# Kernel optimization log

Measured on AMD Instinct MI355X. Metric: run time of the kernel, lower is better.

Reference implementation:

```python
import jax, jax.numpy as jnp
import numpy as np

B, T, C = 4, 2048, 1024
HEAD = 2048

def setup_inputs() -> dict:
    key = jax.random.key(0)
    ks = jax.random.split(key, 7)
    s = 1.0 / np.sqrt(C)
    return {
        "x":  jax.random.normal(ks[0], (B, T, C), dtype=jnp.float32),
        "Wq": jax.random.uniform(ks[1], (C, HEAD), dtype=jnp.float32, minval=-s, maxval=s),
        "bq": jax.random.uniform(ks[2], (HEAD,), dtype=jnp.float32, minval=-s, maxval=s),
        "Wk": jax.random.uniform(ks[3], (C, HEAD), dtype=jnp.float32, minval=-s, maxval=s),
        "bk": jax.random.uniform(ks[4], (HEAD,), dtype=jnp.float32, minval=-s, maxval=s),
        "Wv": jax.random.uniform(ks[5], (C, HEAD), dtype=jnp.float32, minval=-s, maxval=s),
        "bv": jax.random.uniform(ks[6], (HEAD,), dtype=jnp.float32, minval=-s, maxval=s),
    }

def reference(x, Wq, bq, Wk, bk, Wv, bv):
    # q,k,v: [B,T,HEAD]
    q = jnp.einsum('btc,ch->bth', x, Wq) + bq
    k = jnp.einsum('btc,ch->bth', x, Wk) + bk
    v = jnp.einsum('btc,ch->bth', x, Wv) + bv
    scale = x.shape[-1] ** -0.5  # NOTE: original scales by n_embed**-0.5, not head_size
    wei = jnp.einsum('bth,bsh->bts', q, k) * scale  # [B,T,T]
    Tn = x.shape[1]
    causal = jnp.tril(jnp.ones((Tn, Tn), dtype=bool))
    wei = jnp.where(causal, wei, -jnp.inf)
    wei = jax.nn.softmax(wei, axis=-1)
    # dropout is identity in eval mode
    out = jnp.einsum('bts,bsh->bth', wei, v)  # [B,T,HEAD]
    return out
```

## Files before the change

kernel.cpp:

```cpp
#include <hip/hip_runtime.h>


#define T_    2048
#define C_    1024
#define B_    4
#define NQK   4096
#define SCALE 0.03125f

typedef __attribute__((ext_vector_type(4))) float floatx4;
typedef __attribute__((ext_vector_type(8))) short short8;
typedef __attribute__((ext_vector_type(8))) unsigned short ushortx8;

__device__ __forceinline__ unsigned short f2bf(float f) {
  unsigned int u = __float_as_uint(f);
  unsigned int r = (u + 0x7fffu + ((u >> 16) & 1u)) >> 16;
  return (unsigned short)r;
}

__global__ void cast_x_kernel(const float* __restrict__ x, ushort* __restrict__ xbf) {
  int i = blockIdx.x * 256 + threadIdx.x;
  float4 v = ((const float4*)x)[i];
  ushort4 o;
  o.x = f2bf(v.x); o.y = f2bf(v.y); o.z = f2bf(v.z); o.w = f2bf(v.w);
  ((ushort4*)xbf)[i] = o;
}

__global__ void wcast_t_kernel(const float* __restrict__ Wq, const float* __restrict__ Wk,
                               const float* __restrict__ Wv, ushort* __restrict__ WtT) {
  int k0 = blockIdx.x * 32;
  int n0 = blockIdx.y * 32;
  const float* W = (n0 < 2048) ? Wq : (n0 < 4096 ? Wk : Wv);
  int nl0 = n0 & 2047;
  __shared__ ushort tile[32][33];
  int tx = threadIdx.x, ty = threadIdx.y;
  for (int r = ty; r < 32; r += 8)
    tile[r][tx] = f2bf(W[(size_t)(k0 + r) * 2048 + nl0 + tx]);
  __syncthreads();
  for (int r = ty; r < 32; r += 8)
    WtT[(size_t)(n0 + r) * 1024 + k0 + tx] = tile[tx][r];
}

__global__ void bias_cat_kernel(const float* __restrict__ bq, const float* __restrict__ bk,
                                const float* __restrict__ bv, float* __restrict__ bcat) {
  int i = blockIdx.x * 256 + threadIdx.x;
  if (i < 6144) {
    const float* s = (i < 2048) ? bq : (i < 4096 ? bk : bv);
    bcat[i] = s[i & 2047];
  }
}

__device__ __forceinline__ void stage128x32(const ushort* g, int ld, char* lds,
                                            int wave, int lane) {
#pragma unroll
  for (int c = 0; c < 2; ++c) {
    int chunk = wave + 4 * c;
    const ushort* gaddr = g + (size_t)(chunk * 16 + (lane >> 2)) * ld + (lane & 3) * 8;
    char* laddr = lds + chunk * 1024;
    __builtin_amdgcn_global_load_lds((const __attribute__((address_space(1))) unsigned int*)gaddr,
                                     (__attribute__((address_space(3))) unsigned int*)laddr,
                                     16, 0, 0);
  }
}

__device__ __forceinline__ void gemm_core(const ushort* A, int lda,
                                          const ushort* Bm, int ldb, int ksteps,
                                          char* ldsA, char* ldsB, floatx4 acc[4][4]) {
  int tid = threadIdx.x;
  int wave = tid >> 6, lane = tid & 63;
  int wm = wave >> 1, wn = wave & 1;
  int koff2 = ((lane >> 4) * 8) * 2;
  int rbase = lane & 15;
  for (int s = 0; s < ksteps; ++s) {
    __syncthreads();
    stage128x32(A + s * 32, lda, ldsA, wave, lane);
    stage128x32(Bm + s * 32, ldb, ldsB, wave, lane);
    __syncthreads();
    short8 af[4], bf[4];
#pragma unroll
    for (int i = 0; i < 4; ++i) {
      af[i] = *(const short8*)(ldsA + (wm * 64 + i * 16 + rbase) * 64 + koff2);
      bf[i] = *(const short8*)(ldsB + (wn * 64 + i * 16 + rbase) * 64 + koff2);
    }
#pragma unroll
    for (int i = 0; i < 4; ++i)
#pragma unroll
      for (int j = 0; j < 4; ++j)
        acc[i][j] = __builtin_amdgcn_mfma_f32_16x16x32_bf16(af[i], bf[j], acc[i][j], 0, 0, 0);
  }
}


#define MFMA16(a, b, c) __builtin_amdgcn_mfma_f32_16x16x32_bf16((a), (b), (c), 0, 0, 0)

#define GLDS16(gsrc, ldst)                                                                       \
  __builtin_amdgcn_global_load_lds((const __attribute__((address_space(1))) unsigned int*)(gsrc), \
                                   (__attribute__((address_space(3))) unsigned int*)(ldst), 16, 0, 0)
#define STAGE2(gsrc, ldst) do { GLDS16((gsrc), (ldst)); GLDS16((gsrc) + 8192, (ldst) + 1024); } while (0)

#define PHASE_MID() do {                                   \
  __builtin_amdgcn_sched_barrier(0);                       \
  __builtin_amdgcn_s_barrier();                            \
  asm volatile("s_waitcnt lgkmcnt(0)" ::: "memory");       \
  __builtin_amdgcn_sched_barrier(0);                       \
  __builtin_amdgcn_s_setprio(1);                           \
} while (0)

#define PHASE_END() do {                                   \
  __builtin_amdgcn_s_setprio(0);                           \
  __builtin_amdgcn_sched_barrier(0);                       \
  __builtin_amdgcn_s_barrier();                            \
  __builtin_amdgcn_sched_barrier(0);                       \
} while (0)

template <bool TAIL>
__device__ __forceinline__ void iter_qk(const ushort* __restrict__ Ap,
                                        const ushort* __restrict__ Bp,
                                        char* lds, int kt0, int wave, int wm, int wn,
                                        int srcOff, int lnoff0, floatx4 (&acc)[8][4]) {
  char* rA0 = lds + wm * 16384;
  char* rA1 = rA0 + 32768;
  char* rB0 = lds + 65536 + (wn >> 1) * 16384 + (wn & 1) * 8192;
  char* rB1 = rB0 + 32768;
  const ushort* sA1 = Ap + (kt0 + 1) * 64 + srcOff;
  const ushort* sA2 = Ap + (kt0 + 2) * 64 + srcOff;
  const ushort* sB2 = Bp + (kt0 + 2) * 64 + srcOff;
  const ushort* sB3 = Bp + (kt0 + 3) * 64 + srcOff;
  const int lnoff1 = lnoff0 ^ 64;
  short8 af[4][2], blo[2][2], bhi[2][2];

#pragma unroll
  for (int mi = 0; mi < 4; ++mi) {
    af[mi][0] = *(const short8*)(rA0 + mi * 2048 + lnoff0);
    af[mi][1] = *(const short8*)(rA0 + mi * 2048 + lnoff1);
  }
#pragma unroll
  for (int nj = 0; nj < 2; ++nj) {
    blo[nj][0] = *(const short8*)(rB0 + nj * 2048 + lnoff0);
    blo[nj][1] = *(const short8*)(rB0 + nj * 2048 + lnoff1);
  }
  STAGE2(sA1, lds + 32768 + wave * 2048);
  PHASE_MID();
#pragma unroll
  for (int mi = 0; mi < 4; ++mi)
#pragma unroll
    for (int nj = 0; nj < 2; ++nj) {
      acc[mi][nj] = MFMA16(af[mi][0], blo[nj][0], acc[mi][nj]);
      acc[mi][nj] = MFMA16(af[mi][1], blo[nj][1], acc[mi][nj]);
    }
  PHASE_END();

#pragma unroll
  for (int nj = 0; nj < 2; ++nj) {
    bhi[nj][0] = *(const short8*)(rB0 + (2 + nj) * 2048 + lnoff0);
    bhi[nj][1] = *(const short8*)(rB0 + (2 + nj) * 2048 + lnoff1);
  }
  STAGE2(sA1 + 131072, lds + 49152 + wave * 2048);
  PHASE_MID();
#pragma unroll
  for (int mi = 0; mi < 4; ++mi)
#pragma unroll
    for (int nj = 0; nj < 2; ++nj) {
      acc[mi][2 + nj] = MFMA16(af[mi][0], bhi[nj][0], acc[mi][2 + nj]);
      acc[mi][2 + nj] = MFMA16(af[mi][1], bhi[nj][1], acc[mi][2 + nj]);
    }
  PHASE_END();

#pragma unroll
  for (int mi = 0; mi < 4; ++mi) {
    af[mi][0] = *(const short8*)(rA0 + (4 + mi) * 2048 + lnoff0);
    af[mi][1] = *(const short8*)(rA0 + (4 + mi) * 2048 + lnoff1);
  }
  if constexpr (!TAIL) STAGE2(sB2, lds + 65536 + wave * 2048);
  PHASE_MID();
#pragma unroll
  for (int mi = 0; mi < 4; ++mi)
#pragma unroll
    for (int nj = 0; nj < 2; ++nj) {
      acc[4 + mi][2 + nj] = MFMA16(af[mi][0], bhi[nj][0], acc[4 + mi][2 + nj]);
      acc[4 + mi][2 + nj] = MFMA16(af[mi][1], bhi[nj][1], acc[4 + mi][2 + nj]);
    }
  PHASE_END();

  if constexpr (!TAIL) STAGE2(sB2 + 131072, lds + 81920 + wave * 2048);
  PHASE_MID();
#pragma unroll
  for (int mi = 0; mi < 4; ++mi)
#pragma unroll
    for (int nj = 0; nj < 2; ++nj) {
      acc[4 + mi][nj] = MFMA16(af[mi][0], blo[nj][0], acc[4 + mi][nj]);
      acc[4 + mi][nj] = MFMA16(af[mi][1], blo[nj][1], acc[4 + mi][nj]);
    }
  __builtin_amdgcn_s_setprio(0);
  __builtin_amdgcn_sched_barrier(0);
  if constexpr (TAIL) asm volatile("s_waitcnt vmcnt(0)" ::: "memory");
  else                asm volatile("s_waitcnt vmcnt(4)" ::: "memory");
  __builtin_amdgcn_sched_barrier(0);
  __builtin_amdgcn_s_barrier();
  __builtin_amdgcn_sched_barrier(0);

#pragma unroll
  for (int mi = 0; mi < 4; ++mi) {
    af[mi][0] = *(const short8*)(rA1 + mi * 2048 + lnoff0);
    af[mi][1] = *(const short8*)(rA1 + mi * 2048 + lnoff1);
  }
#pragma unroll
  for (int nj = 0; nj < 2; ++nj) {
    blo[nj][0] = *(const short8*)(rB1 + nj * 2048 + lnoff0);
    blo[nj][1] = *(const short8*)(rB1 + nj * 2048 + lnoff1);
  }
  if constexpr (!TAIL) STAGE2(sA2, lds + wave * 2048);
  PHASE_MID();
#pragma unroll
  for (int mi = 0; mi < 4; ++mi)
#pragma unroll
    for (int nj = 0; nj < 2; ++nj) {
      acc[mi][nj] = MFMA16(af[mi][0], blo[nj][0], acc[mi][nj]);
      acc[mi][nj] = MFMA16(af[mi][1], blo[nj][1], acc[mi][nj]);
    }
  PHASE_END();

#pragma unroll
  for (int nj = 0; nj < 2; ++nj) {
    bhi[nj][0] = *(const short8*)(rB1 + (2 + nj) * 2048 + lnoff0);
    bhi[nj][1] = *(const short8*)(rB1 + (2 + nj) * 2048 + lnoff1);
  }
  if constexpr (!TAIL) STAGE2(sA2 + 131072, lds + 16384 + wave * 2048);
  PHASE_MID();
#pragma unroll
  for (int mi = 0; mi < 4; ++mi)
#pragma unroll
    for (int nj = 0; nj < 2; ++nj) {
      acc[mi][2 + nj] = MFMA16(af[mi][0], bhi[nj][0], acc[mi][2 + nj]);
      acc[mi][2 + nj] = MFMA16(af[mi][1], bhi[nj][1], acc[mi][2 + nj]);
    }
  PHASE_END();

#pragma unroll
  for (int mi = 0; mi < 4; ++mi) {
    af[mi][0] = *(const short8*)(rA1 + (4 + mi) * 2048 + lnoff0);
    af[mi][1] = *(const short8*)(rA1 + (4 + mi) * 2048 + lnoff1);
  }
  if constexpr (!TAIL) STAGE2(sB3, lds + 98304 + wave * 2048);
  PHASE_MID();
#pragma unroll
  for (int mi = 0; mi < 4; ++mi)
#pragma unroll
    for (int nj = 0; nj < 2; ++nj) {
      acc[4 + mi][2 + nj] = MFMA16(af[mi][0], bhi[nj][0], acc[4 + mi][2 + nj]);
      acc[4 + mi][2 + nj] = MFMA16(af[mi][1], bhi[nj][1], acc[4 + mi][2 + nj]);
    }
  PHASE_END();

  if constexpr (!TAIL) STAGE2(sB3 + 131072, lds + 114688 + wave * 2048);
  PHASE_MID();
#pragma unroll
  for (int mi = 0; mi < 4; ++mi)
#pragma unroll
    for (int nj = 0; nj < 2; ++nj) {
      acc[4 + mi][nj] = MFMA16(af[mi][0], blo[nj][0], acc[4 + mi][nj]);
      acc[4 + mi][nj] = MFMA16(af[mi][1], blo[nj][1], acc[4 + mi][nj]);
    }
  __builtin_amdgcn_s_setprio(0);
  __builtin_amdgcn_sched_barrier(0);
  if constexpr (!TAIL) asm volatile("s_waitcnt vmcnt(4)" ::: "memory");
  __builtin_amdgcn_sched_barrier(0);
  __builtin_amdgcn_s_barrier();
  __builtin_amdgcn_sched_barrier(0);
}

__global__ __launch_bounds__(512) void gemm_qk256(const ushort* __restrict__ xbf,
                                                  const ushort* __restrict__ WtT,
                                                  const float* __restrict__ bcat,
                                                  ushort* __restrict__ QK) {
  __shared__ __align__(16) char lds[131072];
  int tm = blockIdx.x, tn = blockIdx.y;
  int tid = threadIdx.x;
  int wave = tid >> 6, ln = tid & 63;
  int wm = wave >> 2, wn = wave & 3;
  int ln15 = ln & 15;
  int lnoff0 = ln15 * 128 + (((ln >> 4) * 16) ^ ((ln15 & 7) << 4));
  int srcOff = (wave * 16 + (ln >> 3)) * 1024 + (((ln & 7) * 8) ^ ((ln >> 3) << 3));
  const ushort* Ap = xbf + (size_t)tm * 256 * 1024;
  const ushort* Bp = WtT + (size_t)tn * 256 * 1024;
  floatx4 acc[8][4];
#pragma unroll
  for (int i = 0; i < 8; ++i)
#pragma unroll
    for (int j = 0; j < 4; ++j) acc[i][j] = (floatx4){0.f, 0.f, 0.f, 0.f};

  STAGE2(Ap + srcOff,                 lds + wave * 2048);
  STAGE2(Ap + 131072 + srcOff,        lds + 16384 + wave * 2048);
  STAGE2(Bp + srcOff,                 lds + 65536 + wave * 2048);
  STAGE2(Bp + 131072 + srcOff,        lds + 81920 + wave * 2048);
  STAGE2(Bp + 64 + srcOff,            lds + 98304 + wave * 2048);
  STAGE2(Bp + 64 + 131072 + srcOff,   lds + 114688 + wave * 2048);
  asm volatile("s_waitcnt vmcnt(4)" ::: "memory");
  __builtin_amdgcn_sched_barrier(0);
  __builtin_amdgcn_s_barrier();
  __builtin_amdgcn_sched_barrier(0);

#pragma unroll 1
  for (int i = 0; i < 7; ++i)
    iter_qk<false>(Ap, Bp, lds, 2 * i, wave, wm, wn, srcOff, lnoff0, acc);
  iter_qk<true>(Ap, Bp, lds, 14, wave, wm, wn, srcOff, lnoff0, acc);

  int colb = ln15, rowq = (ln >> 4) * 4;
  int colbase = tn * 256 + wn * 64 + colb;
  float bias[4];
#pragma unroll
  for (int nj = 0; nj < 4; ++nj) bias[nj] = bcat[colbase + nj * 16 - colb + colb];
#pragma unroll
  for (int nj = 0; nj < 4; ++nj) bias[nj] = bcat[tn * 256 + wn * 64 + nj * 16 + colb];
#pragma unroll
  for (int mi = 0; mi < 8; ++mi) {
    int row = tm * 256 + wm * 128 + mi * 16 + rowq;
#pragma unroll
    for (int r = 0; r < 4; ++r) {
      ushort* qrow = QK + (size_t)(row + r) * NQK;
#pragma unroll
      for (int nj = 0; nj < 4; ++nj)
        qrow[colbase + nj * 16] = f2bf(acc[mi][nj][r] + bias[nj]);
    }
  }
}

__global__ __launch_bounds__(256) void gemm_v(const ushort* __restrict__ xbf,
                                              const ushort* __restrict__ WtT,
                                              const float* __restrict__ bcat,
                                              ushort* __restrict__ Vt) {
  __shared__ __align__(16) char lds[128 * 136 * 2];
  char* ldsA = lds;
  char* ldsB = lds + 8192;
  int tm = blockIdx.x, tn = blockIdx.y;
  floatx4 acc[4][4];
#pragma unroll
  for (int i = 0; i < 4; ++i)
#pragma unroll
    for (int j = 0; j < 4; ++j) acc[i][j] = (floatx4){0.f, 0.f, 0.f, 0.f};
  gemm_core(xbf + (size_t)tm * 128 * C_, C_, WtT + (size_t)(32 + tn) * 128 * C_, C_,
            C_ / 32, ldsA, ldsB, acc);
  int tid = threadIdx.x, wave = tid >> 6, lane = tid & 63;
  int wm = wave >> 1, wn = wave & 1;
  int colb = lane & 15, rowq = (lane >> 4) * 4;
  __syncthreads();
  ushort* tileT = (ushort*)lds;
#pragma unroll
  for (int j = 0; j < 4; ++j) {
    int h = wn * 64 + j * 16 + colb;
    float bv = bcat[4096 + tn * 128 + h];
#pragma unroll
    for (int i = 0; i < 4; ++i) {
      int s = wm * 64 + i * 16 + rowq;
      ushort4 o4;
      o4.x = f2bf(acc[i][j][0] + bv);
      o4.y = f2bf(acc[i][j][1] + bv);
      o4.z = f2bf(acc[i][j][2] + bv);
      o4.w = f2bf(acc[i][j][3] + bv);
      *(ushort4*)(tileT + h * 136 + s) = o4;
    }
  }
  __syncthreads();
  int b = tm >> 4, sbase = (tm & 15) * 128;
  int hr = tid >> 4, sc = (tid & 15) * 8;
#pragma unroll
  for (int it = 0; it < 8; ++it) {
    int h = it * 16 + hr;
    ushortx8 v = *(const ushortx8*)(tileT + h * 136 + sc);
    *(ushortx8*)(Vt + ((size_t)b * T_ + tn * 128 + h) * T_ + sbase + sc) = v;
  }
}

__global__ __launch_bounds__(256) void gemm_s(const ushort* __restrict__ QK,
                                              float* __restrict__ S) {
  int l = blockIdx.x, b = blockIdx.y;
  int tm = (int)((sqrtf(8.f * l + 1.f) - 1.f) * 0.5f);
  while ((tm + 1) * (tm + 2) / 2 <= l) ++tm;
  while (tm * (tm + 1) / 2 > l) --tm;
  int tn = l - tm * (tm + 1) / 2;
  __shared__ __align__(16) char ldsA[8192], ldsB[8192];
  floatx4 acc[4][4];
#pragma unroll
  for (int i = 0; i < 4; ++i)
#pragma unroll
    for (int j = 0; j < 4; ++j) acc[i][j] = (floatx4){0.f, 0.f, 0.f, 0.f};
  const ushort* Ab = QK + (size_t)b * T_ * NQK + (size_t)tm * 128 * NQK;
  const ushort* Bb = QK + (size_t)b * T_ * NQK + (size_t)tn * 128 * NQK + 2048;
  gemm_core(Ab, NQK, Bb, NQK, T_ / 32, ldsA, ldsB, acc);
  float* Sb = S + (size_t)b * T_ * T_;
  int tid = threadIdx.x, wave = tid >> 6, lane = tid & 63;
  int wm = wave >> 1, wn = wave & 1;
  int colb = lane & 15, rowq = (lane >> 4) * 4;
#pragma unroll
  for (int i = 0; i < 4; ++i) {
    int row = tm * 128 + wm * 64 + i * 16 + rowq;
#pragma unroll
    for (int j = 0; j < 4; ++j) {
      int col = tn * 128 + wn * 64 + j * 16 + colb;
#pragma unroll
      for (int r = 0; r < 4; ++r)
        Sb[(size_t)(row + r) * T_ + col] = acc[i][j][r] * SCALE;
    }
  }
}

__global__ __launch_bounds__(256) void softmax_causal(const float* __restrict__ S,
                                                      ushort* __restrict__ P) {
  int t = blockIdx.x, b = blockIdx.y;
  int tid = threadIdx.x;
  const float* srow = S + ((size_t)b * T_ + t) * T_;
  ushort* prow = P + ((size_t)b * T_ + t) * T_;
  int band = ((t >> 7) + 1) << 7;
  float xv[8];
  float m = -INFINITY;
#pragma unroll
  for (int c = 0; c < 2; ++c) {
    int s0 = c * 1024 + tid * 4;
    float* xs = xv + c * 4;
    if (s0 < band) {
      float4 v = *(const float4*)(srow + s0);
      xs[0] = (s0 + 0 <= t) ? v.x : -INFINITY;
      xs[1] = (s0 + 1 <= t) ? v.y : -INFINITY;
      xs[2] = (s0 + 2 <= t) ? v.z : -INFINITY;
      xs[3] = (s0 + 3 <= t) ? v.w : -INFINITY;
      m = fmaxf(fmaxf(fmaxf(xs[0], xs[1]), fmaxf(xs[2], xs[3])), m);
    } else {
      xs[0] = xs[1] = xs[2] = xs[3] = -INFINITY;
    }
  }
  __shared__ float sm4[4];
  int wid = tid >> 6, ln = tid & 63;
#pragma unroll
  for (int o = 32; o; o >>= 1) m = fmaxf(m, __shfl_xor(m, o));
  if (ln == 0) sm4[wid] = m;
  __syncthreads();
  m = fmaxf(fmaxf(sm4[0], sm4[1]), fmaxf(sm4[2], sm4[3]));
  __syncthreads();
  float sum = 0.f;
#pragma unroll
  for (int k = 0; k < 8; ++k) { xv[k] = __expf(xv[k] - m); sum += xv[k]; }
#pragma unroll
  for (int o = 32; o; o >>= 1) sum += __shfl_xor(sum, o);
  if (ln == 0) sm4[wid] = sum;
  __syncthreads();
  sum = sm4[0] + sm4[1] + sm4[2] + sm4[3];
  float inv = 1.0f / sum;
#pragma unroll
  for (int c = 0; c < 2; ++c) {
    int s0 = c * 1024 + tid * 4;
    if (s0 < band) {
      ushort4 o4;
      o4.x = f2bf(xv[c * 4 + 0] * inv);
      o4.y = f2bf(xv[c * 4 + 1] * inv);
      o4.z = f2bf(xv[c * 4 + 2] * inv);
      o4.w = f2bf(xv[c * 4 + 3] * inv);
      *(ushort4*)(prow + s0) = o4;
    }
  }
}

__global__ __launch_bounds__(256) void gemm_o(const ushort* __restrict__ P,
                                              const ushort* __restrict__ Vt,
                                              float* __restrict__ O) {
  int tn = blockIdx.x, tm = 15 - blockIdx.y, b = blockIdx.z;
  __shared__ __align__(16) char ldsA[8192], ldsB[8192];
  floatx4 acc[4][4];
#pragma unroll
  for (int i = 0; i < 4; ++i)
#pragma unroll
    for (int j = 0; j < 4; ++j) acc[i][j] = (floatx4){0.f, 0.f, 0.f, 0.f};
  const ushort* Ab = P + (size_t)b * T_ * T_ + (size_t)tm * 128 * T_;
  const ushort* Bb = Vt + (size_t)b * T_ * T_ + (size_t)tn * 128 * T_;
  gemm_core(Ab, T_, Bb, T_, (tm + 1) * 4, ldsA, ldsB, acc);
  float* Ob = O + (size_t)b * T_ * T_;
  int tid = threadIdx.x, wave = tid >> 6, lane = tid & 63;
  int wm = wave >> 1, wn = wave & 1;
  int colb = lane & 15, rowq = (lane >> 4) * 4;
#pragma unroll
  for (int i = 0; i < 4; ++i) {
    int row = tm * 128 + wm * 64 + i * 16 + rowq;
#pragma unroll
    for (int j = 0; j < 4; ++j) {
      int col = tn * 128 + wn * 64 + j * 16 + colb;
#pragma unroll
      for (int r = 0; r < 4; ++r)
        Ob[(size_t)(row + r) * T_ + col] = acc[i][j][r];
    }
  }
}

extern "C" void kernel_launch(void* const* d_in, const int* in_sizes, int n_in,
                              void* d_out, int out_size, void* d_ws, size_t ws_size,
                              hipStream_t stream) {
  (void)in_sizes; (void)n_in; (void)out_size; (void)ws_size;
  const float* x  = (const float*)d_in[0];
  const float* Wq = (const float*)d_in[1];
  const float* bq = (const float*)d_in[2];
  const float* Wk = (const float*)d_in[3];
  const float* bk = (const float*)d_in[4];
  const float* Wv = (const float*)d_in[5];
  const float* bv = (const float*)d_in[6];

  char* ws = (char*)d_ws;
  ushort* xbf  = (ushort*)(ws + 0);
  ushort* WtT  = (ushort*)(ws + 16777216);
  float*  bcat = (float*) (ws + 29360128);
  ushort* QK   = (ushort*)(ws + 29384704);
  ushort* P    = (ushort*)(ws + 96493568);
  ushort* Vt   = (ushort*)(ws + 130048000);

  float* S = (float*)d_out;
  float* O = (float*)d_out;

  cast_x_kernel  <<<8192, 256, 0, stream>>>(x, xbf);
  wcast_t_kernel <<<dim3(32, 192), dim3(32, 8), 0, stream>>>(Wq, Wk, Wv, WtT);
  bias_cat_kernel<<<24, 256, 0, stream>>>(bq, bk, bv, bcat);
  gemm_qk256     <<<dim3(32, 16), 512, 0, stream>>>(xbf, WtT, bcat, QK);
  gemm_v         <<<dim3(64, 16), 256, 0, stream>>>(xbf, WtT, bcat, Vt);
  gemm_s         <<<dim3(136, 4), 256, 0, stream>>>(QK, S);
  softmax_causal <<<dim3(2048, 4), 256, 0, stream>>>(S, P);
  gemm_o         <<<dim3(16, 16, 4), 256, 0, stream>>>(P, Vt, O);
}
```

Before: 410.8 us.

## Port S and O GEMMs to the pipelined 256x256 tile kernel

Generalizes the tuned 256x256, 512-thread, LDS-pipelined QK projection mainloop over leading dimensions and uses it for the causal score GEMM and the P·V GEMM, replacing 128x128 gemm_core kernels. The softmax causal band is widened to 256-granularity to match the new tiles. Larger tiles raise arithmetic intensity and reuse the hand-scheduled direct-to-LDS loads. In exchange, grids shrink (144 and 256 blocks), which risks under-filling the GPU, and more masked work is done near the causal diagonal.

```diff
diff --git a/kernel.cpp b/kernel.cpp
--- a/kernel.cpp
+++ b/kernel.cpp
@@ -95,7 +95,12 @@
 #define GLDS16(gsrc, ldst)                                                                       \
   __builtin_amdgcn_global_load_lds((const __attribute__((address_space(1))) unsigned int*)(gsrc), \
                                    (__attribute__((address_space(3))) unsigned int*)(ldst), 16, 0, 0)
-#define STAGE2(gsrc, ldst) do { GLDS16((gsrc), (ldst)); GLDS16((gsrc) + 8192, (ldst) + 1024); } while (0)
+
+template <int LD>
+__device__ __forceinline__ void stage_half(const ushort* gsrc, char* ldst) {
+  GLDS16(gsrc, ldst);
+  GLDS16(gsrc + 8 * LD, ldst + 1024);
+}
 
 #define PHASE_MID() do {                                   \
   __builtin_amdgcn_sched_barrier(0);                       \
@@ -112,19 +117,35 @@
   __builtin_amdgcn_sched_barrier(0);                       \
 } while (0)
 
-template <bool TAIL>
-__device__ __forceinline__ void iter_qk(const ushort* __restrict__ Ap,
+template <int LDA, int LDB>
+__device__ __forceinline__ void prologue256(const ushort* Ap, const ushort* Bp,
+                                            char* lds, int wave, int srcOffA, int srcOffB) {
+  stage_half<LDA>(Ap + srcOffA,                     lds + wave * 2048);
+  stage_half<LDA>(Ap + 128 * LDA + srcOffA,         lds + 16384 + wave * 2048);
+  stage_half<LDB>(Bp + srcOffB,                     lds + 65536 + wave * 2048);
+  stage_half<LDB>(Bp + 128 * LDB + srcOffB,         lds + 81920 + wave * 2048);
+  stage_half<LDB>(Bp + 64 + srcOffB,                lds + 98304 + wave * 2048);
+  stage_half<LDB>(Bp + 64 + 128 * LDB + srcOffB,    lds + 114688 + wave * 2048);
+  asm volatile("s_waitcnt vmcnt(4)" ::: "memory");
+  __builtin_amdgcn_sched_barrier(0);
+  __builtin_amdgcn_s_barrier();
+  __builtin_amdgcn_sched_barrier(0);
+}
+
+template <int LDA, int LDB, bool TAIL>
+__device__ __forceinline__ void iter256(const ushort* __restrict__ Ap,
                                         const ushort* __restrict__ Bp,
                                         char* lds, int kt0, int wave, int wm, int wn,
-                                        int srcOff, int lnoff0, floatx4 (&acc)[8][4]) {
+                                        int srcOffA, int srcOffB, int lnoff0,
+                                        floatx4 (&acc)[8][4]) {
   char* rA0 = lds + wm * 16384;
   char* rA1 = rA0 + 32768;
   char* rB0 = lds + 65536 + (wn >> 1) * 16384 + (wn & 1) * 8192;
   char* rB1 = rB0 + 32768;
-  const ushort* sA1 = Ap + (kt0 + 1) * 64 + srcOff;
-  const ushort* sA2 = Ap + (kt0 + 2) * 64 + srcOff;
-  const ushort* sB2 = Bp + (kt0 + 2) * 64 + srcOff;
-  const ushort* sB3 = Bp + (kt0 + 3) * 64 + srcOff;
+  const ushort* sA1 = Ap + (kt0 + 1) * 64 + srcOffA;
+  const ushort* sA2 = Ap + (kt0 + 2) * 64 + srcOffA;
+  const ushort* sB2 = Bp + (kt0 + 2) * 64 + srcOffB;
+  const ushort* sB3 = Bp + (kt0 + 3) * 64 + srcOffB;
   const int lnoff1 = lnoff0 ^ 64;
   short8 af[4][2], blo[2][2], bhi[2][2];
 
@@ -138,7 +159,7 @@
     blo[nj][0] = *(const short8*)(rB0 + nj * 2048 + lnoff0);
     blo[nj][1] = *(const short8*)(rB0 + nj * 2048 + lnoff1);
   }
-  STAGE2(sA1, lds + 32768 + wave * 2048);
+  stage_half<LDA>(sA1, lds + 32768 + wave * 2048);
   PHASE_MID();
 #pragma unroll
   for (int mi = 0; mi < 4; ++mi)
@@ -154,7 +175,7 @@
     bhi[nj][0] = *(const short8*)(rB0 + (2 + nj) * 2048 + lnoff0);
     bhi[nj][1] = *(const short8*)(rB0 + (2 + nj) * 2048 + lnoff1);
   }
-  STAGE2(sA1 + 131072, lds + 49152 + wave * 2048);
+  stage_half<LDA>(sA1 + 128 * LDA, lds + 49152 + wave * 2048);
   PHASE_MID();
 #pragma unroll
   for (int mi = 0; mi < 4; ++mi)
@@ -170,7 +191,7 @@
     af[mi][0] = *(const short8*)(rA0 + (4 + mi) * 2048 + lnoff0);
     af[mi][1] = *(const short8*)(rA0 + (4 + mi) * 2048 + lnoff1);
   }
-  if constexpr (!TAIL) STAGE2(sB2, lds + 65536 + wave * 2048);
+  if constexpr (!TAIL) stage_half<LDB>(sB2, lds + 65536 + wave * 2048);
   PHASE_MID();
 #pragma unroll
   for (int mi = 0; mi < 4; ++mi)
@@ -181,7 +202,7 @@
     }
   PHASE_END();
 
-  if constexpr (!TAIL) STAGE2(sB2 + 131072, lds + 81920 + wave * 2048);
+  if constexpr (!TAIL) stage_half<LDB>(sB2 + 128 * LDB, lds + 81920 + wave * 2048);
   PHASE_MID();
 #pragma unroll
   for (int mi = 0; mi < 4; ++mi)
@@ -208,7 +229,7 @@
     blo[nj][0] = *(const short8*)(rB1 + nj * 2048 + lnoff0);
     blo[nj][1] = *(const short8*)(rB1 + nj * 2048 + lnoff1);
   }
-  if constexpr (!TAIL) STAGE2(sA2, lds + wave * 2048);
+  if constexpr (!TAIL) stage_half<LDA>(sA2, lds + wave * 2048);
   PHASE_MID();
 #pragma unroll
   for (int mi = 0; mi < 4; ++mi)
@@ -224,7 +245,7 @@
     bhi[nj][0] = *(const short8*)(rB1 + (2 + nj) * 2048 + lnoff0);
     bhi[nj][1] = *(const short8*)(rB1 + (2 + nj) * 2048 + lnoff1);
   }
-  if constexpr (!TAIL) STAGE2(sA2 + 131072, lds + 16384 + wave * 2048);
+  if constexpr (!TAIL) stage_half<LDA>(sA2 + 128 * LDA, lds + 16384 + wave * 2048);
   PHASE_MID();
 #pragma unroll
   for (int mi = 0; mi < 4; ++mi)
@@ -240,7 +261,7 @@
     af[mi][0] = *(const short8*)(rA1 + (4 + mi) * 2048 + lnoff0);
     af[mi][1] = *(const short8*)(rA1 + (4 + mi) * 2048 + lnoff1);
   }
-  if constexpr (!TAIL) STAGE2(sB3, lds + 98304 + wave * 2048);
+  if constexpr (!TAIL) stage_half<LDB>(sB3, lds + 98304 + wave * 2048);
   PHASE_MID();
 #pragma unroll
   for (int mi = 0; mi < 4; ++mi)
@@ -251,7 +272,7 @@
     }
   PHASE_END();
 
-  if constexpr (!TAIL) STAGE2(sB3 + 131072, lds + 114688 + wave * 2048);
+  if constexpr (!TAIL) stage_half<LDB>(sB3 + 128 * LDB, lds + 114688 + wave * 2048);
   PHASE_MID();
 #pragma unroll
   for (int mi = 0; mi < 4; ++mi)
@@ -266,6 +287,23 @@
   __builtin_amdgcn_sched_barrier(0);
   __builtin_amdgcn_s_barrier();
   __builtin_amdgcn_sched_barrier(0);
+}
+
+struct Addr256 {
+  int wave, wm, wn, ln, ln15, lnoff0;
+};
+__device__ __forceinline__ Addr256 addr256() {
+  Addr256 a;
+  int tid = threadIdx.x;
+  a.wave = tid >> 6; a.ln = tid & 63;
+  a.wm = a.wave >> 2; a.wn = a.wave & 3;
+  a.ln15 = a.ln & 15;
+  a.lnoff0 = a.ln15 * 128 + (((a.ln >> 4) * 16) ^ ((a.ln15 & 7) << 4));
+  return a;
+}
+template <int LD>
+__device__ __forceinline__ int srcOff256(int wave, int ln) {
+  return (wave * 16 + (ln >> 3)) * LD + (((ln & 7) * 8) ^ ((ln >> 3) << 3));
 }
 
 __global__ __launch_bounds__(512) void gemm_qk256(const ushort* __restrict__ xbf,
@@ -274,12 +312,8 @@
                                                   ushort* __restrict__ QK) {
   __shared__ __align__(16) char lds[131072];
   int tm = blockIdx.x, tn = blockIdx.y;
-  int tid = threadIdx.x;
-  int wave = tid >> 6, ln = tid & 63;
-  int wm = wave >> 2, wn = wave & 3;
-  int ln15 = ln & 15;
-  int lnoff0 = ln15 * 128 + (((ln >> 4) * 16) ^ ((ln15 & 7) << 4));
-  int srcOff = (wave * 16 + (ln >> 3)) * 1024 + (((ln & 7) * 8) ^ ((ln >> 3) << 3));
+  Addr256 a = addr256();
+  int srcOff = srcOff256<1024>(a.wave, a.ln);
   const ushort* Ap = xbf + (size_t)tm * 256 * 1024;
   const ushort* Bp = WtT + (size_t)tn * 256 * 1024;
   floatx4 acc[8][4];
@@ -288,38 +322,104 @@
 #pragma unroll
     for (int j = 0; j < 4; ++j) acc[i][j] = (floatx4){0.f, 0.f, 0.f, 0.f};
 
-  STAGE2(Ap + srcOff,                 lds + wave * 2048);
-  STAGE2(Ap + 131072 + srcOff,        lds + 16384 + wave * 2048);
-  STAGE2(Bp + srcOff,                 lds + 65536 + wave * 2048);
-  STAGE2(Bp + 131072 + srcOff,        lds + 81920 + wave * 2048);
-  STAGE2(Bp + 64 + srcOff,            lds + 98304 + wave * 2048);
-  STAGE2(Bp + 64 + 131072 + srcOff,   lds + 114688 + wave * 2048);
-  asm volatile("s_waitcnt vmcnt(4)" ::: "memory");
-  __builtin_amdgcn_sched_barrier(0);
-  __builtin_amdgcn_s_barrier();
-  __builtin_amdgcn_sched_barrier(0);
-
+  prologue256<1024, 1024>(Ap, Bp, lds, a.wave, srcOff, srcOff);
 #pragma unroll 1
   for (int i = 0; i < 7; ++i)
-    iter_qk<false>(Ap, Bp, lds, 2 * i, wave, wm, wn, srcOff, lnoff0, acc);
-  iter_qk<true>(Ap, Bp, lds, 14, wave, wm, wn, srcOff, lnoff0, acc);
-
-  int colb = ln15, rowq = (ln >> 4) * 4;
-  int colbase = tn * 256 + wn * 64 + colb;
+    iter256<1024, 1024, false>(Ap, Bp, lds, 2 * i, a.wave, a.wm, a.wn, srcOff, srcOff, a.lnoff0, acc);
+  iter256<1024, 1024, true>(Ap, Bp, lds, 14, a.wave, a.wm, a.wn, srcOff, srcOff, a.lnoff0, acc);
+
+  int colb = a.ln15, rowq = (a.ln >> 4) * 4;
+  int colbase = tn * 256 + a.wn * 64 + colb;
   float bias[4];
 #pragma unroll
-  for (int nj = 0; nj < 4; ++nj) bias[nj] = bcat[colbase + nj * 16 - colb + colb];
-#pragma unroll
-  for (int nj = 0; nj < 4; ++nj) bias[nj] = bcat[tn * 256 + wn * 64 + nj * 16 + colb];
+  for (int nj = 0; nj < 4; ++nj) bias[nj] = bcat[colbase + nj * 16];
 #pragma unroll
   for (int mi = 0; mi < 8; ++mi) {
-    int row = tm * 256 + wm * 128 + mi * 16 + rowq;
+    int row = tm * 256 + a.wm * 128 + mi * 16 + rowq;
 #pragma unroll
     for (int r = 0; r < 4; ++r) {
       ushort* qrow = QK + (size_t)(row + r) * NQK;
 #pragma unroll
       for (int nj = 0; nj < 4; ++nj)
         qrow[colbase + nj * 16] = f2bf(acc[mi][nj][r] + bias[nj]);
+    }
+  }
+}
+
+__global__ __launch_bounds__(512) void gemm_s256(const ushort* __restrict__ QK,
+                                                 float* __restrict__ S) {
+  int l = blockIdx.x, b = blockIdx.y;
+  int tm = (int)((sqrtf(8.f * l + 1.f) - 1.f) * 0.5f);
+  while ((tm + 1) * (tm + 2) / 2 <= l) ++tm;
+  while (tm * (tm + 1) / 2 > l) --tm;
+  int tn = l - tm * (tm + 1) / 2;
+  __shared__ __align__(16) char lds[131072];
+  Addr256 a = addr256();
+  int srcOff = srcOff256<NQK>(a.wave, a.ln);
+  const ushort* Ap = QK + (size_t)b * T_ * NQK + (size_t)tm * 256 * NQK;
+  const ushort* Bp = QK + (size_t)b * T_ * NQK + (size_t)tn * 256 * NQK + 2048;
+  floatx4 acc[8][4];
+#pragma unroll
+  for (int i = 0; i < 8; ++i)
+#pragma unroll
+    for (int j = 0; j < 4; ++j) acc[i][j] = (floatx4){0.f, 0.f, 0.f, 0.f};
+
+  prologue256<NQK, NQK>(Ap, Bp, lds, a.wave, srcOff, srcOff);
+#pragma unroll 1
+  for (int i = 0; i < 15; ++i)
+    iter256<NQK, NQK, false>(Ap, Bp, lds, 2 * i, a.wave, a.wm, a.wn, srcOff, srcOff, a.lnoff0, acc);
+  iter256<NQK, NQK, true>(Ap, Bp, lds, 30, a.wave, a.wm, a.wn, srcOff, srcOff, a.lnoff0, acc);
+
+  float* Sb = S + (size_t)b * T_ * T_;
+  int colb = a.ln15, rowq = (a.ln >> 4) * 4;
+  int colbase = tn * 256 + a.wn * 64 + colb;
+#pragma unroll
+  for (int mi = 0; mi < 8; ++mi) {
+    int row = tm * 256 + a.wm * 128 + mi * 16 + rowq;
+#pragma unroll
+    for (int r = 0; r < 4; ++r) {
+      float* srow = Sb + (size_t)(row + r) * T_;
+#pragma unroll
+      for (int nj = 0; nj < 4; ++nj)
+        srow[colbase + nj * 16] = acc[mi][nj][r] * SCALE;
+    }
+  }
+}
+
+__global__ __launch_bounds__(512) void gemm_o256(const ushort* __restrict__ P,
+                                                 const ushort* __restrict__ Vt,
+                                                 float* __restrict__ O) {
+  int tn = blockIdx.x, tm = 7 - blockIdx.y, b = blockIdx.z;
+  __shared__ __align__(16) char lds[131072];
+  Addr256 a = addr256();
+  int srcOff = srcOff256<T_>(a.wave, a.ln);
+  const ushort* Ap = P + (size_t)b * T_ * T_ + (size_t)tm * 256 * T_;
+  const ushort* Bp = Vt + (size_t)b * T_ * T_ + (size_t)tn * 256 * T_;
+  floatx4 acc[8][4];
+#pragma unroll
+  for (int i = 0; i < 8; ++i)
+#pragma unroll
+    for (int j = 0; j < 4; ++j) acc[i][j] = (floatx4){0.f, 0.f, 0.f, 0.f};
+
+  int niter = (tm + 1) * 2;
+  prologue256<T_, T_>(Ap, Bp, lds, a.wave, srcOff, srcOff);
+#pragma unroll 1
+  for (int i = 0; i < niter - 1; ++i)
+    iter256<T_, T_, false>(Ap, Bp, lds, 2 * i, a.wave, a.wm, a.wn, srcOff, srcOff, a.lnoff0, acc);
+  iter256<T_, T_, true>(Ap, Bp, lds, 2 * (niter - 1), a.wave, a.wm, a.wn, srcOff, srcOff, a.lnoff0, acc);
+
+  float* Ob = O + (size_t)b * T_ * T_;
+  int colb = a.ln15, rowq = (a.ln >> 4) * 4;
+  int colbase = tn * 256 + a.wn * 64 + colb;
+#pragma unroll
+  for (int mi = 0; mi < 8; ++mi) {
+    int row = tm * 256 + a.wm * 128 + mi * 16 + rowq;
+#pragma unroll
+    for (int r = 0; r < 4; ++r) {
+      float* orow = Ob + (size_t)(row + r) * T_;
+#pragma unroll
+      for (int nj = 0; nj < 4; ++nj)
+        orow[colbase + nj * 16] = acc[mi][nj][r];
     }
   }
 }
@@ -370,46 +470,13 @@
   }
 }
 
-__global__ __launch_bounds__(256) void gemm_s(const ushort* __restrict__ QK,
-                                              float* __restrict__ S) {
-  int l = blockIdx.x, b = blockIdx.y;
-  int tm = (int)((sqrtf(8.f * l + 1.f) - 1.f) * 0.5f);
-  while ((tm + 1) * (tm + 2) / 2 <= l) ++tm;
-  while (tm * (tm + 1) / 2 > l) --tm;
-  int tn = l - tm * (tm + 1) / 2;
-  __shared__ __align__(16) char ldsA[8192], ldsB[8192];
-  floatx4 acc[4][4];
-#pragma unroll
-  for (int i = 0; i < 4; ++i)
-#pragma unroll
-    for (int j = 0; j < 4; ++j) acc[i][j] = (floatx4){0.f, 0.f, 0.f, 0.f};
-  const ushort* Ab = QK + (size_t)b * T_ * NQK + (size_t)tm * 128 * NQK;
-  const ushort* Bb = QK + (size_t)b * T_ * NQK + (size_t)tn * 128 * NQK + 2048;
-  gemm_core(Ab, NQK, Bb, NQK, T_ / 32, ldsA, ldsB, acc);
-  float* Sb = S + (size_t)b * T_ * T_;
-  int tid = threadIdx.x, wave = tid >> 6, lane = tid & 63;
-  int wm = wave >> 1, wn = wave & 1;
-  int colb = lane & 15, rowq = (lane >> 4) * 4;
-#pragma unroll
-  for (int i = 0; i < 4; ++i) {
-    int row = tm * 128 + wm * 64 + i * 16 + rowq;
-#pragma unroll
-    for (int j = 0; j < 4; ++j) {
-      int col = tn * 128 + wn * 64 + j * 16 + colb;
-#pragma unroll
-      for (int r = 0; r < 4; ++r)
-        Sb[(size_t)(row + r) * T_ + col] = acc[i][j][r] * SCALE;
-    }
-  }
-}
-
 __global__ __launch_bounds__(256) void softmax_causal(const float* __restrict__ S,
                                                       ushort* __restrict__ P) {
   int t = blockIdx.x, b = blockIdx.y;
   int tid = threadIdx.x;
   const float* srow = S + ((size_t)b * T_ + t) * T_;
   ushort* prow = P + ((size_t)b * T_ + t) * T_;
-  int band = ((t >> 7) + 1) << 7;
+  int band = ((t >> 8) + 1) << 8;
   float xv[8];
   float m = -INFINITY;
 #pragma unroll
@@ -458,36 +525,6 @@
   }
 }
 
-__global__ __launch_bounds__(256) void gemm_o(const ushort* __restrict__ P,
-                                              const ushort* __restrict__ Vt,
-                                              float* __restrict__ O) {
-  int tn = blockIdx.x, tm = 15 - blockIdx.y, b = blockIdx.z;
-  __shared__ __align__(16) char ldsA[8192], ldsB[8192];
-  floatx4 acc[4][4];
-#pragma unroll
-  for (int i = 0; i < 4; ++i)
-#pragma unroll
-    for (int j = 0; j < 4; ++j) acc[i][j] = (floatx4){0.f, 0.f, 0.f, 0.f};
-  const ushort* Ab = P + (size_t)b * T_ * T_ + (size_t)tm * 128 * T_;
-  const ushort* Bb = Vt + (size_t)b * T_ * T_ + (size_t)tn * 128 * T_;
-  gemm_core(Ab, T_, Bb, T_, (tm + 1) * 4, ldsA, ldsB, acc);
-  float* Ob = O + (size_t)b * T_ * T_;
-  int tid = threadIdx.x, wave = tid >> 6, lane = tid & 63;
-  int wm = wave >> 1, wn = wave & 1;
-  int colb = lane & 15, rowq = (lane >> 4) * 4;
-#pragma unroll
-  for (int i = 0; i < 4; ++i) {
-    int row = tm * 128 + wm * 64 + i * 16 + rowq;
-#pragma unroll
-    for (int j = 0; j < 4; ++j) {
-      int col = tn * 128 + wn * 64 + j * 16 + colb;
-#pragma unroll
-      for (int r = 0; r < 4; ++r)
-        Ob[(size_t)(row + r) * T_ + col] = acc[i][j][r];
-    }
-  }
-}
-
 extern "C" void kernel_launch(void* const* d_in, const int* in_sizes, int n_in,
                               void* d_out, int out_size, void* d_ws, size_t ws_size,
                               hipStream_t stream) {
@@ -516,7 +553,7 @@
   bias_cat_kernel<<<24, 256, 0, stream>>>(bq, bk, bv, bcat);
   gemm_qk256     <<<dim3(32, 16), 512, 0, stream>>>(xbf, WtT, bcat, QK);
   gemm_v         <<<dim3(64, 16), 256, 0, stream>>>(xbf, WtT, bcat, Vt);
-  gemm_s         <<<dim3(136, 4), 256, 0, stream>>>(QK, S);
+  gemm_s256      <<<dim3(36, 4), 512, 0, stream>>>(QK, S);
   softmax_causal <<<dim3(2048, 4), 256, 0, stream>>>(S, P);
-  gemm_o         <<<dim3(16, 16, 4), 256, 0, stream>>>(P, Vt, O);
-}
+  gemm_o256      <<<dim3(8, 8, 4), 512, 0, stream>>>(P, Vt, O);
+}
```

Measured after the change: 360.0 us. 12.4% less time.
